# Performance work log

Hardware: AMD Instinct MI355X
Metric: run time of the kernel (lower is better)

Reference implementation:

```python
import jax, jax.numpy as jnp
import numpy as np

L_MAX = 3
N_MAX = 8
N_PSEUDO = 4
N_SPECIES = 4
CUTOFF = 5.0


def real_sph_harm(u):
    # u: [E,3] unit vectors -> real spherical harmonics, l=0..3, [E,16]
    x, y, z = u[:, 0], u[:, 1], u[:, 2]
    x2, y2, z2 = x * x, y * y, z * z
    Y = [
        0.28209479177387814 * jnp.ones_like(x),
        0.4886025119029199 * y,
        0.4886025119029199 * z,
        0.4886025119029199 * x,
        1.0925484305920792 * x * y,
        1.0925484305920792 * y * z,
        0.31539156525252005 * (3.0 * z2 - 1.0),
        1.0925484305920792 * x * z,
        0.5462742152960396 * (x2 - y2),
        0.5900435899266435 * y * (3.0 * x2 - y2),
        2.890611442640554 * x * y * z,
        0.4570457994644658 * y * (5.0 * z2 - 1.0),
        0.3731763325901154 * z * (5.0 * z2 - 3.0),
        0.4570457994644658 * x * (5.0 * z2 - 1.0),
        1.445305721320277 * z * (x2 - y2),
        0.5900435899266435 * x * (x2 - 3.0 * y2),
    ]
    return jnp.stack(Y, axis=-1)


def setup_inputs() -> dict:
    key = jax.random.key(0)
    k0, k1, k2, k3 = jax.random.split(key, 4)
    N, E = 20000, 320000
    positions = jax.random.normal(k0, (N, 3), jnp.float32) * 2.0
    cells = (30.0 * jnp.eye(3, dtype=jnp.float32))[None]  # [1,3,3]
    species = jax.random.randint(k1, (N,), 0, N_SPECIES)  # species indices
    edge_indices = jax.random.randint(k2, (2, E), 0, N)
    edge_shifts = jnp.zeros((E, 3), jnp.int32)
    species_embed = jax.random.normal(k3, (N_SPECIES, N_PSEUDO), jnp.float32)  # alchemical coupling
    radial_mu = jnp.linspace(0.0, CUTOFF, N_MAX).astype(jnp.float32)
    radial_sigma = jnp.full((1,), 0.6, jnp.float32)
    return {
        "positions": positions,
        "cells": cells,
        "species": species,
        "edge_indices": edge_indices,
        "edge_shifts": edge_shifts,
        "species_embed": species_embed,
        "radial_mu": radial_mu,
        "radial_sigma": radial_sigma,
    }


def reference(positions, cells, species, edge_indices, edge_shifts, species_embed, radial_mu, radial_sigma):
    i, j = edge_indices[0], edge_indices[1]
    # per-edge displacement with periodic shifts
    rij = positions[j] - positions[i] + edge_shifts.astype(positions.dtype) @ cells[0]  # [E,3]
    r = jnp.sqrt(jnp.sum(rij * rij, axis=-1) + 1e-12)  # [E]
    u = rij / r[:, None]
    # smooth cosine cutoff
    fcut = jnp.where(r < CUTOFF, 0.5 * (jnp.cos(jnp.pi * r / CUTOFF) + 1.0), 0.0)
    # radial expansion [E, n_max]
    sig = radial_sigma[0]
    R = jnp.exp(-((r[:, None] - radial_mu) ** 2) / (2.0 * sig * sig)) * fcut[:, None]
    # angular expansion [E, (l_max+1)^2]
    Y = real_sph_harm(u)
    # alchemical pseudo-species embedding of the neighbor species [E, P]
    ej = species_embed[species[j]]
    N = positions.shape[0]
    outs = []
    for l in range(L_MAX + 1):
        Yl = Y[:, l * l:(l + 1) * (l + 1)]  # [E, 2l+1]
        # per-edge spherical-expansion contribution, properties = (pseudo, n) flattened -> Q
        feat = jnp.einsum('em,ep,en->empn', Yl, ej, R).reshape(Yl.shape[0], 2 * l + 1, -1)
        # scatter edges to centers: c_{i,m,q}
        c = jax.ops.segment_sum(feat, i, num_segments=N)  # [N, 2l+1, Q]
        cg = (2 * l + 1) ** (-0.5)
        # power spectrum: cg * sum_m c_{imq} c_{imr}  -> [N, Q, Q]
        ps = cg * jnp.einsum('nmq,nmr->nqr', c, c)
        outs.append(ps.reshape(N, -1))
    return jnp.concatenate(outs, axis=-1)  # [N, sum_l Q^2] = [20000, 4096]
```

## Files before the change

kernel.cpp:

```cpp
#include <hip/hip_runtime.h>
#include <math.h>

#define NM       16
#define NQ       32
#define CUT      5.0f
#define CAP      96
#define CHUNK    16
#define SLOT     52

typedef float v4f __attribute__((ext_vector_type(4)));

__global__ __launch_bounds__(256) void edge_bin_kernel(
    const float* __restrict__ pos,
    const float* __restrict__ cells,
    const int*   __restrict__ species,
    const int*   __restrict__ eidx,
    const int*   __restrict__ eshift,
    int*         __restrict__ counts,
    float4*      __restrict__ buckets,
    int E)
{
    const int e = blockIdx.x * blockDim.x + threadIdx.x;
    if (e >= E) return;

    const int i = eidx[e];
    const int j = eidx[E + e];

    float dx = pos[3 * j + 0] - pos[3 * i + 0];
    float dy = pos[3 * j + 1] - pos[3 * i + 1];
    float dz = pos[3 * j + 2] - pos[3 * i + 2];

    const int sx = eshift[3 * e + 0];
    const int sy = eshift[3 * e + 1];
    const int sz = eshift[3 * e + 2];
    dx += (float)sx * cells[0] + (float)sy * cells[3] + (float)sz * cells[6];
    dy += (float)sx * cells[1] + (float)sy * cells[4] + (float)sz * cells[7];
    dz += (float)sx * cells[2] + (float)sy * cells[5] + (float)sz * cells[8];

    const float r2 = dx * dx + dy * dy + dz * dz;
    if (r2 >= CUT * CUT) return;

    const int slot = atomicAdd(&counts[i], 1);
    if (slot < CAP)
        buckets[(size_t)i * CAP + slot] =
            make_float4(dx, dy, dz, __int_as_float(species[j]));
}

__global__ __launch_bounds__(256) void node_fused_kernel(
    const float4* __restrict__ buckets,
    const int*    __restrict__ counts,
    const float*  __restrict__ semb,
    const float*  __restrict__ mu,
    const float*  __restrict__ sigma,
    float*        __restrict__ out,
    int N)
{
    const int wid  = threadIdx.x >> 6;
    const int lane = threadIdx.x & 63;
    const int node = blockIdx.x * 4 + wid;
    if (node >= N) return;

    __shared__ __align__(16) float sE[4][CHUNK * SLOT];
    float* wbase = sE[wid];

    const float sig    = sigma[0];
    const float inv2s2 = -1.0f / (2.0f * sig * sig);

    const int cnt = min(counts[node], CAP);

    const int q = lane & 31;
    const int h = lane >> 5;
    v4f acc0 = {0.f, 0.f, 0.f, 0.f};
    v4f acc1 = {0.f, 0.f, 0.f, 0.f};

    for (int base = 0; base < cnt; base += CHUNK) {
        const int nb = min(cnt - base, CHUNK);

        if (lane < nb) {
            const float4 b = buckets[(size_t)node * CAP + base + lane];
            const float dx = b.x, dy = b.y, dz = b.z;
            const float r2 = dx * dx + dy * dy + dz * dz + 1e-12f;
            const float r  = sqrtf(r2);
            const float invr = 1.0f / r;
            const float x = dx * invr, y = dy * invr, z = dz * invr;
            const float x2 = x * x, y2 = y * y, z2 = z * z;

            v4f* slot4 = (v4f*)(wbase + lane * SLOT);
            v4f Ya, Yb, Yc, Yd;
            Ya[0] = 0.28209479177387814f;
            Ya[1] = 0.4886025119029199f * y;
            Ya[2] = 0.4886025119029199f * z;
            Ya[3] = 0.4886025119029199f * x;
            Yb[0] = 1.0925484305920792f * x * y;
            Yb[1] = 1.0925484305920792f * y * z;
            Yb[2] = 0.31539156525252005f * (3.0f * z2 - 1.0f);
            Yb[3] = 1.0925484305920792f * x * z;
            Yc[0] = 0.5462742152960396f * (x2 - y2);
            Yc[1] = 0.5900435899266435f * y * (3.0f * x2 - y2);
            Yc[2] = 2.890611442640554f  * x * y * z;
            Yc[3] = 0.4570457994644658f * y * (5.0f * z2 - 1.0f);
            Yd[0] = 0.3731763325901154f * z * (5.0f * z2 - 3.0f);
            Yd[1] = 0.4570457994644658f * x * (5.0f * z2 - 1.0f);
            Yd[2] = 1.445305721320277f  * z * (x2 - y2);
            Yd[3] = 0.5900435899266435f * x * (x2 - 3.0f * y2);
            slot4[0] = Ya; slot4[1] = Yb; slot4[2] = Yc; slot4[3] = Yd;

            const float fcut = 0.5f * (__cosf(0.62831853071795864f * r) + 1.0f);
            float Rf[8];
#pragma unroll
            for (int n = 0; n < 8; ++n) {
                const float dr = r - mu[n];
                Rf[n] = __expf(dr * dr * inv2s2) * fcut;
            }
            const int sj = __float_as_int(b.w);
#pragma unroll
            for (int p = 0; p < 4; ++p) {
                const float ejp = semb[sj * 4 + p];
                v4f w0, w1;
#pragma unroll
                for (int n = 0; n < 4; ++n) { w0[n] = ejp * Rf[n]; w1[n] = ejp * Rf[4 + n]; }
                slot4[4 + 2 * p]     = w0;
                slot4[4 + 2 * p + 1] = w1;
            }
        }

        for (int e = 0; e < nb; ++e) {
            const float* ed = wbase + e * SLOT;
            const float w  = ed[16 + q];
            const v4f y0 = *(const v4f*)(ed + h * 8);
            const v4f y1 = *(const v4f*)(ed + h * 8 + 4);
            acc0 += y0 * w;
            acc1 += y1 * w;
        }
    }

    float* wc = wbase;
#pragma unroll
    for (int jj = 0; jj < 4; ++jj) {
        wc[(h * 8 + jj) * NQ + q]     = acc0[jj];
        wc[(h * 8 + 4 + jj) * NQ + q] = acc1[jj];
    }

    const float cg[4] = {1.0f, 0.57735026918962576f,
                         0.44721359549995794f, 0.37796447300922723f};
    const v4f* wc4 = (const v4f*)wbase;
    const int  r4  = lane & 7;
    const int  qh  = lane >> 3;
    v4f* op = (v4f*)out + (size_t)node * 1024;

#pragma unroll
    for (int l = 0; l < 4; ++l) {
        const int mb = l * l;
        const int mc = 2 * l + 1;
        v4f bv[7];
#pragma unroll
        for (int m = 0; m < 7; ++m)
            if (m < mc) bv[m] = wc4[(mb + m) * 8 + r4];
        const float cgl = cg[l];
#pragma unroll
        for (int k = 0; k < 4; ++k) {
            const int q2 = k * 8 + qh;
            v4f s = {0.f, 0.f, 0.f, 0.f};
#pragma unroll
            for (int m = 0; m < 7; ++m)
                if (m < mc) s += wc[(mb + m) * NQ + q2] * bv[m];
            s *= cgl;
            __builtin_nontemporal_store(s, &op[l * 256 + k * 64 + lane]);
        }
    }
}

extern "C" void kernel_launch(void* const* d_in, const int* in_sizes, int n_in,
                              void* d_out, int out_size, void* d_ws, size_t ws_size,
                              hipStream_t stream) {
    const float* pos     = (const float*)d_in[0];
    const float* cells   = (const float*)d_in[1];
    const int*   species = (const int*)  d_in[2];
    const int*   eidx    = (const int*)  d_in[3];
    const int*   eshift  = (const int*)  d_in[4];
    const float* semb    = (const float*)d_in[5];
    const float* mu      = (const float*)d_in[6];
    const float* sigma   = (const float*)d_in[7];
    float*       out     = (float*)d_out;

    const int N = in_sizes[0] / 3;
    const int E = in_sizes[3] / 2;

    float4* buckets = (float4*)d_ws;
    const size_t bucket_bytes = (size_t)N * CAP * sizeof(float4);
    int* counts = (int*)((char*)d_ws + bucket_bytes);

    hipMemsetAsync(counts, 0, (size_t)N * sizeof(int), stream);

    edge_bin_kernel<<<(E + 255) / 256, 256, 0, stream>>>(
        pos, cells, species, eidx, eshift, counts, buckets, E);

    node_fused_kernel<<<(N + 3) / 4, 256, 0, stream>>>(
        buckets, counts, semb, mu, sigma, out, N);
}
```

Measured before the change: 367.0 us.

## Move per-edge feature computation into edge kernel, gather by edge id in node kernel

The spherical-harmonic, radial and species-embedding features are now computed once per surviving edge in the edge kernel, with all lanes busy, and written to a global feature array indexed by edge id. Buckets store edge ids instead of displacement vectors. The node kernel gathers features straight from global memory, two edges per iteration, with no shared-memory staging or intra-wave idle lanes. This adds a large global write and read of 48 floats per edge plus scattered gathers, in exchange for removing divergence and the serial chunked compute in the node kernel.

```diff
diff --git a/kernel.cpp b/kernel.cpp
--- a/kernel.cpp
+++ b/kernel.cpp
@@ -5,19 +5,22 @@
 #define NQ       32
 #define CUT      5.0f
 #define CAP      96
-#define CHUNK    16
-#define SLOT     52
+#define FSTRIDE  48
 
 typedef float v4f __attribute__((ext_vector_type(4)));
 
-__global__ __launch_bounds__(256) void edge_bin_kernel(
+__global__ __launch_bounds__(256) void edge_feat_kernel(
     const float* __restrict__ pos,
     const float* __restrict__ cells,
     const int*   __restrict__ species,
     const int*   __restrict__ eidx,
     const int*   __restrict__ eshift,
+    const float* __restrict__ semb,
+    const float* __restrict__ mu,
+    const float* __restrict__ sigma,
     int*         __restrict__ counts,
-    float4*      __restrict__ buckets,
+    int*         __restrict__ ids,
+    float*       __restrict__ feat,
     int E)
 {
     const int e = blockIdx.x * blockDim.x + threadIdx.x;
@@ -41,100 +44,105 @@
     if (r2 >= CUT * CUT) return;
 
     const int slot = atomicAdd(&counts[i], 1);
-    if (slot < CAP)
-        buckets[(size_t)i * CAP + slot] =
-            make_float4(dx, dy, dz, __int_as_float(species[j]));
+    if (slot >= CAP) return;
+    ids[(size_t)i * CAP + slot] = e;
+
+    const float r    = sqrtf(r2 + 1e-12f);
+    const float invr = 1.0f / r;
+    const float x = dx * invr, y = dy * invr, z = dz * invr;
+    const float x2 = x * x, y2 = y * y, z2 = z * z;
+
+    v4f* fp = (v4f*)(feat + (size_t)e * FSTRIDE);
+
+    v4f Ya, Yb, Yc, Yd;
+    Ya[0] = 0.28209479177387814f;
+    Ya[1] = 0.4886025119029199f * y;
+    Ya[2] = 0.4886025119029199f * z;
+    Ya[3] = 0.4886025119029199f * x;
+    Yb[0] = 1.0925484305920792f * x * y;
+    Yb[1] = 1.0925484305920792f * y * z;
+    Yb[2] = 0.31539156525252005f * (3.0f * z2 - 1.0f);
+    Yb[3] = 1.0925484305920792f * x * z;
+    Yc[0] = 0.5462742152960396f * (x2 - y2);
+    Yc[1] = 0.5900435899266435f * y * (3.0f * x2 - y2);
+    Yc[2] = 2.890611442640554f  * x * y * z;
+    Yc[3] = 0.4570457994644658f * y * (5.0f * z2 - 1.0f);
+    Yd[0] = 0.3731763325901154f * z * (5.0f * z2 - 3.0f);
+    Yd[1] = 0.4570457994644658f * x * (5.0f * z2 - 1.0f);
+    Yd[2] = 1.445305721320277f  * z * (x2 - y2);
+    Yd[3] = 0.5900435899266435f * x * (x2 - 3.0f * y2);
+    fp[0] = Ya; fp[1] = Yb; fp[2] = Yc; fp[3] = Yd;
+
+    const float sig    = sigma[0];
+    const float inv2s2 = -1.0f / (2.0f * sig * sig);
+    const float fcut   = 0.5f * (__cosf(0.62831853071795864f * r) + 1.0f);
+
+    float Rf[8];
+#pragma unroll
+    for (int n = 0; n < 8; ++n) {
+        const float dr = r - mu[n];
+        Rf[n] = __expf(dr * dr * inv2s2) * fcut;
+    }
+    const int sj = species[j];
+#pragma unroll
+    for (int p = 0; p < 4; ++p) {
+        const float ejp = semb[sj * 4 + p];
+        v4f w0, w1;
+#pragma unroll
+        for (int n = 0; n < 4; ++n) { w0[n] = ejp * Rf[n]; w1[n] = ejp * Rf[4 + n]; }
+        fp[4 + 2 * p]     = w0;
+        fp[4 + 2 * p + 1] = w1;
+    }
 }
 
-__global__ __launch_bounds__(256) void node_fused_kernel(
-    const float4* __restrict__ buckets,
-    const int*    __restrict__ counts,
-    const float*  __restrict__ semb,
-    const float*  __restrict__ mu,
-    const float*  __restrict__ sigma,
-    float*        __restrict__ out,
+__global__ __launch_bounds__(256) void node_ps_kernel(
+    const float* __restrict__ feat,
+    const int*   __restrict__ ids,
+    const int*   __restrict__ counts,
+    float*       __restrict__ out,
     int N)
 {
     const int wid  = threadIdx.x >> 6;
     const int lane = threadIdx.x & 63;
     const int node = blockIdx.x * 4 + wid;
+
+    __shared__ __align__(16) float sc[4][NM * NQ];
+    float* wc = sc[wid];
+
     if (node >= N) return;
 
-    __shared__ __align__(16) float sE[4][CHUNK * SLOT];
-    float* wbase = sE[wid];
-
-    const float sig    = sigma[0];
-    const float inv2s2 = -1.0f / (2.0f * sig * sig);
-
     const int cnt = min(counts[node], CAP);
-
     const int q = lane & 31;
     const int h = lane >> 5;
+    const int* myids = ids + (size_t)node * CAP;
+
     v4f acc0 = {0.f, 0.f, 0.f, 0.f};
     v4f acc1 = {0.f, 0.f, 0.f, 0.f};
 
-    for (int base = 0; base < cnt; base += CHUNK) {
-        const int nb = min(cnt - base, CHUNK);
-
-        if (lane < nb) {
-            const float4 b = buckets[(size_t)node * CAP + base + lane];
-            const float dx = b.x, dy = b.y, dz = b.z;
-            const float r2 = dx * dx + dy * dy + dz * dz + 1e-12f;
-            const float r  = sqrtf(r2);
-            const float invr = 1.0f / r;
-            const float x = dx * invr, y = dy * invr, z = dz * invr;
-            const float x2 = x * x, y2 = y * y, z2 = z * z;
-
-            v4f* slot4 = (v4f*)(wbase + lane * SLOT);
-            v4f Ya, Yb, Yc, Yd;
-            Ya[0] = 0.28209479177387814f;
-            Ya[1] = 0.4886025119029199f * y;
-            Ya[2] = 0.4886025119029199f * z;
-            Ya[3] = 0.4886025119029199f * x;
-            Yb[0] = 1.0925484305920792f * x * y;
-            Yb[1] = 1.0925484305920792f * y * z;
-            Yb[2] = 0.31539156525252005f * (3.0f * z2 - 1.0f);
-            Yb[3] = 1.0925484305920792f * x * z;
-            Yc[0] = 0.5462742152960396f * (x2 - y2);
-            Yc[1] = 0.5900435899266435f * y * (3.0f * x2 - y2);
-            Yc[2] = 2.890611442640554f  * x * y * z;
-            Yc[3] = 0.4570457994644658f * y * (5.0f * z2 - 1.0f);
-            Yd[0] = 0.3731763325901154f * z * (5.0f * z2 - 3.0f);
-            Yd[1] = 0.4570457994644658f * x * (5.0f * z2 - 1.0f);
-            Yd[2] = 1.445305721320277f  * z * (x2 - y2);
-            Yd[3] = 0.5900435899266435f * x * (x2 - 3.0f * y2);
-            slot4[0] = Ya; slot4[1] = Yb; slot4[2] = Yc; slot4[3] = Yd;
-
-            const float fcut = 0.5f * (__cosf(0.62831853071795864f * r) + 1.0f);
-            float Rf[8];
-#pragma unroll
-            for (int n = 0; n < 8; ++n) {
-                const float dr = r - mu[n];
-                Rf[n] = __expf(dr * dr * inv2s2) * fcut;
-            }
-            const int sj = __float_as_int(b.w);
-#pragma unroll
-            for (int p = 0; p < 4; ++p) {
-                const float ejp = semb[sj * 4 + p];
-                v4f w0, w1;
-#pragma unroll
-                for (int n = 0; n < 4; ++n) { w0[n] = ejp * Rf[n]; w1[n] = ejp * Rf[4 + n]; }
-                slot4[4 + 2 * p]     = w0;
-                slot4[4 + 2 * p + 1] = w1;
-            }
-        }
-
-        for (int e = 0; e < nb; ++e) {
-            const float* ed = wbase + e * SLOT;
-            const float w  = ed[16 + q];
-            const v4f y0 = *(const v4f*)(ed + h * 8);
-            const v4f y1 = *(const v4f*)(ed + h * 8 + 4);
-            acc0 += y0 * w;
-            acc1 += y1 * w;
-        }
-    }
-
-    float* wc = wbase;
+    int k = 0;
+    for (; k + 2 <= cnt; k += 2) {
+        const int e0 = myids[k];
+        const int e1 = myids[k + 1];
+        const float* f0 = feat + (size_t)e0 * FSTRIDE;
+        const float* f1 = feat + (size_t)e1 * FSTRIDE;
+        const float w0 = f0[16 + q];
+        const float w1 = f1[16 + q];
+        const v4f y00 = *(const v4f*)(f0 + h * 8);
+        const v4f y01 = *(const v4f*)(f0 + h * 8 + 4);
+        const v4f y10 = *(const v4f*)(f1 + h * 8);
+        const v4f y11 = *(const v4f*)(f1 + h * 8 + 4);
+        acc0 += y00 * w0; acc1 += y01 * w0;
+        acc0 += y10 * w1; acc1 += y11 * w1;
+    }
+    if (k < cnt) {
+        const int e0 = myids[k];
+        const float* f0 = feat + (size_t)e0 * FSTRIDE;
+        const float w0 = f0[16 + q];
+        const v4f y00 = *(const v4f*)(f0 + h * 8);
+        const v4f y01 = *(const v4f*)(f0 + h * 8 + 4);
+        acc0 += y00 * w0; acc1 += y01 * w0;
+    }
+
 #pragma unroll
     for (int jj = 0; jj < 4; ++jj) {
         wc[(h * 8 + jj) * NQ + q]     = acc0[jj];
@@ -143,7 +151,7 @@
 
     const float cg[4] = {1.0f, 0.57735026918962576f,
                          0.44721359549995794f, 0.37796447300922723f};
-    const v4f* wc4 = (const v4f*)wbase;
+    const v4f* wc4 = (const v4f*)wc;
     const int  r4  = lane & 7;
     const int  qh  = lane >> 3;
     v4f* op = (v4f*)out + (size_t)node * 1024;
@@ -158,14 +166,14 @@
             if (m < mc) bv[m] = wc4[(mb + m) * 8 + r4];
         const float cgl = cg[l];
 #pragma unroll
-        for (int k = 0; k < 4; ++k) {
-            const int q2 = k * 8 + qh;
+        for (int kk = 0; kk < 4; ++kk) {
+            const int q2 = kk * 8 + qh;
             v4f s = {0.f, 0.f, 0.f, 0.f};
 #pragma unroll
             for (int m = 0; m < 7; ++m)
                 if (m < mc) s += wc[(mb + m) * NQ + q2] * bv[m];
             s *= cgl;
-            __builtin_nontemporal_store(s, &op[l * 256 + k * 64 + lane]);
+            __builtin_nontemporal_store(s, &op[l * 256 + kk * 64 + lane]);
         }
     }
 }
@@ -186,15 +194,18 @@
     const int N = in_sizes[0] / 3;
     const int E = in_sizes[3] / 2;
 
-    float4* buckets = (float4*)d_ws;
-    const size_t bucket_bytes = (size_t)N * CAP * sizeof(float4);
-    int* counts = (int*)((char*)d_ws + bucket_bytes);
+    float* feat = (float*)d_ws;
+    size_t off  = (size_t)E * FSTRIDE * sizeof(float);
+    int* ids    = (int*)((char*)d_ws + off);
+    off += (size_t)N * CAP * sizeof(int);
+    int* counts = (int*)((char*)d_ws + off);
 
     hipMemsetAsync(counts, 0, (size_t)N * sizeof(int), stream);
 
-    edge_bin_kernel<<<(E + 255) / 256, 256, 0, stream>>>(
-        pos, cells, species, eidx, eshift, counts, buckets, E);
-
-    node_fused_kernel<<<(N + 3) / 4, 256, 0, stream>>>(
-        buckets, counts, semb, mu, sigma, out, N);
+    edge_feat_kernel<<<(E + 255) / 256, 256, 0, stream>>>(
+        pos, cells, species, eidx, eshift, semb, mu, sigma,
+        counts, ids, feat, E);
+
+    node_ps_kernel<<<(N + 3) / 4, 256, 0, stream>>>(
+        feat, ids, counts, out, N);
 }
```

Measured after the change: 405.8 us. 1.11x slower.
